# Kernel optimization log

Measured on AMD Instinct MI355X. Metric: run time of the kernel, lower is better.

## Reference

```python
import jax, jax.numpy as jnp
import numpy as np

B, M, D, H = 2, 2048, 1024, 16
DH = D // H            # 64 head dim
FF = 2624              # GeGLU intermediate size
EPS = 1e-5
ROPE_BASE = 10000.0


def _layernorm(x, g, b):
    mu = jnp.mean(x, axis=-1, keepdims=True)
    var = jnp.mean(jnp.square(x - mu), axis=-1, keepdims=True)
    return (x - mu) * jax.lax.rsqrt(var + EPS) * g + b


def _rope_cos_sin(m, dh):
    # HF-style: inv_freq over even dims; only first dh/2 entries are used by apply_rope
    inv_freq = 1.0 / (ROPE_BASE ** (jnp.arange(0, dh, 2, dtype=jnp.float32) / dh))  # [dh/2]
    ang = jnp.arange(m, dtype=jnp.float32)[:, None] * inv_freq[None, :]             # [M, dh/2]
    return jnp.cos(ang), jnp.sin(ang)


def _apply_rope(x, c, s):
    # x: [B,H,M,dh]; c,s: [M,dh/2] broadcast over B,H. Half-split (non-interleaved) rotation.
    x1, x2 = jnp.split(x, 2, axis=-1)
    return jnp.concatenate([x1 * c - x2 * s, x1 * s + x2 * c], axis=-1)


def setup_inputs() -> dict:
    key = jax.random.key(0)
    ks = jax.random.split(key, 6)
    w = lambda k, shape: (jax.random.normal(k, shape, jnp.float32) * 0.02)
    return {
        "hidden_states": jax.random.normal(ks[0], (B, M, D), jnp.float32),
        "attention_mask": jnp.ones((B, M), jnp.int32),
        "ln1_g": jnp.ones((D,), jnp.float32),
        "ln1_b": jnp.zeros((D,), jnp.float32),
        "Wqkv_w": w(ks[1], (3 * D, D)),
        "Wqkv_b": jnp.zeros((3 * D,), jnp.float32),
        "Wo_w": w(ks[2], (D, D)),
        "ln2_g": jnp.ones((D,), jnp.float32),
        "ln2_b": jnp.zeros((D,), jnp.float32),
        "Wi_w": w(ks[3], (2 * FF, D)),
        "Wmlp_o_w": w(ks[4], (D, FF)),
    }


def reference(hidden_states, attention_mask, ln1_g, ln1_b, Wqkv_w, Wqkv_b, Wo_w,
              ln2_g, ln2_b, Wi_w, Wmlp_o_w):
    x = hidden_states                                    # [B,M,D]
    xn = _layernorm(x, ln1_g, ln1_b)
    qkv = xn @ Wqkv_w.T + Wqkv_b                         # [B,M,3D]
    qkv = qkv.reshape(B, M, 3, H, DH).transpose(0, 3, 1, 2, 4)  # [B,H,M,3,dh]
    q, k, v = qkv[..., 0, :], qkv[..., 1, :], qkv[..., 2, :]    # each [B,H,M,dh]

    c, s = _rope_cos_sin(M, DH)                          # [M, dh/2]
    q = _apply_rope(q, c, s)
    k = _apply_rope(k, c, s)

    scale = 1.0 / np.sqrt(DH)
    scores = jnp.einsum("bhmd,bhnd->bhmn", q, k) * scale  # [B,H,M,M]
    keep = (attention_mask > 0)[:, None, None, :]         # [B,1,1,M] padding mask on keys
    scores = jnp.where(keep, scores, -jnp.inf)
    p = jax.nn.softmax(scores, axis=-1)
    o = jnp.einsum("bhmn,bhnd->bhmd", p, v)               # [B,H,M,dh]

    attn_out = o.transpose(0, 2, 1, 3).reshape(B, M, D)
    x = x + attn_out @ Wo_w.T

    # ModernBERT GeGLU MLP: input, gate = Wi(x).chunk(2); Wo(gelu(input) * gate)
    xn2 = _layernorm(x, ln2_g, ln2_b)
    hg = xn2 @ Wi_w.T                                     # [B,M,2*FF]
    h_in, h_gate = jnp.split(hg, 2, axis=-1)
    x = x + (jax.nn.gelu(h_in) * h_gate) @ Wmlp_o_w.T
    return x
```

## Files before the change

kernel.cpp:

```cpp
#include <hip/hip_runtime.h>
#include <cstdint>
#include <cstddef>

using u16 = unsigned short;
using u32 = uint32_t;

typedef __attribute__((ext_vector_type(8))) short short8;
typedef __attribute__((ext_vector_type(4))) float floatx4;

#define DEVFN static __device__ __forceinline__

#define QSCALE 0.18033688011112042f

DEVFN u16 f2bf(float f) {
  u32 u = __float_as_uint(f);
  return (u16)((u + 0x7fffu + ((u >> 16) & 1u)) >> 16);
}

DEVFN float b2f(u16 u) { return __uint_as_float(((u32)u) << 16); }

DEVFN void async_load16(const void* g, const void* lds) {
  __builtin_amdgcn_global_load_lds(
      (const __attribute__((address_space(1))) u32*)(uintptr_t)g,
      (__attribute__((address_space(3))) u32*)(u32)(uintptr_t)lds,
      16, 0, 0);
}

DEVFN void cvt4(const float* __restrict__ src, u16* __restrict__ dst, int i) {
  const float4 v = ((const float4*)src)[i];
  ushort4 o;
  o.x = f2bf(v.x); o.y = f2bf(v.y); o.z = f2bf(v.z); o.w = f2bf(v.w);
  ((ushort4*)dst)[i] = o;
}

__global__ __launch_bounds__(256)
void prep_k(const float* __restrict__ Wqkv, const float* __restrict__ Wo,
            const float* __restrict__ Wi, const float* __restrict__ Wmlp,
            const float* __restrict__ hidden, const float* __restrict__ ln1g,
            const float* __restrict__ ln1b,
            u16* __restrict__ wqkv_bf, u16* __restrict__ wo_bf,
            u16* __restrict__ wi_bf, u16* __restrict__ wmlp_bf,
            float* __restrict__ ct, float* __restrict__ st, u16* __restrict__ xn) {
  const int bid = blockIdx.x;
  const int tid = threadIdx.x;
  __shared__ float red[8];
  if (bid < 256) {
    const int i = bid * 256 + tid;
    const int m = i >> 5, f = i & 31;
    const float inv = exp2f((float)f * -0.41524101186092025f);
    const float ang = (float)m * inv;
    ct[i] = cosf(ang);
    st[i] = sinf(ang);
  } else if (bid < 3328) {
    cvt4(Wqkv, wqkv_bf, (bid - 256) * 256 + tid);
  } else if (bid < 4352) {
    cvt4(Wo, wo_bf, (bid - 3328) * 256 + tid);
  } else if (bid < 9600) {
    const int i = (bid - 4352) * 256 + tid;
    const int i4 = i * 4;
    const int p = i4 >> 10, kc = i4 & 1023;
    const int g = p >> 5, c = p & 31;
    const int srow = (c < 16) ? (g * 16 + c) : (2624 + g * 16 + (c - 16));
    const float4 v = *(const float4*)(Wi + (size_t)srow * 1024 + kc);
    ushort4 o;
    o.x = f2bf(v.x); o.y = f2bf(v.y); o.z = f2bf(v.z); o.w = f2bf(v.w);
    ((ushort4*)wi_bf)[i] = o;
  } else if (bid < 12224) {
    cvt4(Wmlp, wmlp_bf, (bid - 9600) * 256 + tid);
  } else {
    const int row = bid - 12224;
    const float4 v = ((const float4*)(hidden + (size_t)row * 1024))[tid];
    float s = v.x + v.y + v.z + v.w;
    float ss = v.x * v.x + v.y * v.y + v.z * v.z + v.w * v.w;
#pragma unroll
    for (int d = 32; d > 0; d >>= 1) {
      s += __shfl_xor(s, d);
      ss += __shfl_xor(ss, d);
    }
    const int wave = tid >> 6;
    if ((tid & 63) == 0) { red[wave] = s; red[4 + wave] = ss; }
    __syncthreads();
    s = red[0] + red[1] + red[2] + red[3];
    ss = red[4] + red[5] + red[6] + red[7];
    const float mu = s * (1.f / 1024.f);
    const float var = ss * (1.f / 1024.f) - mu * mu;
    const float rr = rsqrtf(var + 1e-5f);
    const float4 gv = ((const float4*)ln1g)[tid];
    const float4 bv = ((const float4*)ln1b)[tid];
    u16* orow = xn + (size_t)row * 1024 + tid * 4;
    orow[0] = f2bf((v.x - mu) * rr * gv.x + bv.x);
    orow[1] = f2bf((v.y - mu) * rr * gv.y + bv.y);
    orow[2] = f2bf((v.z - mu) * rr * gv.z + bv.z);
    orow[3] = f2bf((v.w - mu) * rr * gv.w + bv.w);
  }
}

__global__ __launch_bounds__(256)
void red_ln_k(const float* __restrict__ resid, const u16* __restrict__ p0,
              const u16* __restrict__ p1, const u16* __restrict__ p2,
              const float* __restrict__ g, const float* __restrict__ bb,
              float* __restrict__ outx, u16* __restrict__ outn) {
  const int row = blockIdx.x;
  const int tid = threadIdx.x;
  const size_t base = (size_t)row * 1024;
  const float4 h = ((const float4*)(resid + base))[tid];
  const ushort4 a = ((const ushort4*)(p0 + base))[tid];
  const ushort4 c = ((const ushort4*)(p1 + base))[tid];
  const ushort4 d = ((const ushort4*)(p2 + base))[tid];
  float4 v;
  v.x = h.x + b2f(a.x) + b2f(c.x) + b2f(d.x);
  v.y = h.y + b2f(a.y) + b2f(c.y) + b2f(d.y);
  v.z = h.z + b2f(a.z) + b2f(c.z) + b2f(d.z);
  v.w = h.w + b2f(a.w) + b2f(c.w) + b2f(d.w);
  float s = v.x + v.y + v.z + v.w;
  float ss = v.x * v.x + v.y * v.y + v.z * v.z + v.w * v.w;
#pragma unroll
  for (int dd = 32; dd > 0; dd >>= 1) {
    s += __shfl_xor(s, dd);
    ss += __shfl_xor(ss, dd);
  }
  __shared__ float red[8];
  const int wave = tid >> 6;
  if ((tid & 63) == 0) { red[wave] = s; red[4 + wave] = ss; }
  __syncthreads();
  s = red[0] + red[1] + red[2] + red[3];
  ss = red[4] + red[5] + red[6] + red[7];
  const float mu = s * (1.f / 1024.f);
  const float var = ss * (1.f / 1024.f) - mu * mu;
  const float rr = rsqrtf(var + 1e-5f);
  ((float4*)(outx + base))[tid] = v;
  const float4 gv = ((const float4*)g)[tid];
  const float4 bv = ((const float4*)bb)[tid];
  u16* orow = outn + base + tid * 4;
  orow[0] = f2bf((v.x - mu) * rr * gv.x + bv.x);
  orow[1] = f2bf((v.y - mu) * rr * gv.y + bv.y);
  orow[2] = f2bf((v.z - mu) * rr * gv.z + bv.z);
  orow[3] = f2bf((v.w - mu) * rr * gv.w + bv.w);
}

__global__ void red_add_k(float* __restrict__ out, const u16* __restrict__ p0,
                          const u16* __restrict__ p1, const u16* __restrict__ p2,
                          const u16* __restrict__ p3) {
  const int i = blockIdx.x * 256 + threadIdx.x;
  float4 v = ((const float4*)out)[i];
  const ushort4 a = ((const ushort4*)p0)[i];
  const ushort4 c = ((const ushort4*)p1)[i];
  const ushort4 d = ((const ushort4*)p2)[i];
  const ushort4 e = ((const ushort4*)p3)[i];
  v.x += b2f(a.x) + b2f(c.x) + b2f(d.x) + b2f(e.x);
  v.y += b2f(a.y) + b2f(c.y) + b2f(d.y) + b2f(e.y);
  v.z += b2f(a.z) + b2f(c.z) + b2f(d.z) + b2f(e.z);
  v.w += b2f(a.w) + b2f(c.w) + b2f(d.w) + b2f(e.w);
  ((float4*)out)[i] = v;
}

DEVFN void swizzle_tile(int NT, int& tn, int& tm) {
  const int tpx = gridDim.x >> 3;
  const int p = blockIdx.x;
  const int lid = (p & 7) * tpx + (p >> 3);
  const int band = lid / (8 * NT);
  const int rem = lid - band * 8 * NT;
  tn = (rem >> 3) * 128;
  tm = (band * 8 + (rem & 7)) * 128;
}

struct EpiArgs {
  const float* bias;
  u16* q; u16* kk; u16* vt;
  u16* outbf;
  const float* ct; const float* st;
};

template <int EPI>
__global__ __launch_bounds__(256, 3)
void gemm_k(const u16* __restrict__ A, const u16* __restrict__ B, int K, int NT,
            EpiArgs ea) {
  __shared__ __align__(16) u16 sA[128 * 32];
  __shared__ __align__(16) u16 sB[128 * 32];
  int tn, tm;
  swizzle_tile(NT, tn, tm);
  const int tid = threadIdx.x;
  const int wave = tid >> 6, lane = tid & 63;
  const int quad = lane >> 4, l15 = lane & 15;
  const int wm = (wave >> 1) * 64, wn = (wave & 1) * 64;

  floatx4 acc[4][4];
#pragma unroll
  for (int i = 0; i < 4; ++i)
#pragma unroll
    for (int j = 0; j < 4; ++j) acc[i][j] = (floatx4){0.f, 0.f, 0.f, 0.f};

  const int srow = lane >> 2;
  const int skc = (lane & 3) * 8;
  const u16* sAr = sA + (wm + l15) * 32 + quad * 8;
  const u16* sBr = sB + (wn + l15) * 32 + quad * 8;

  for (int k0 = 0; k0 < K; k0 += 32) {
#pragma unroll
    for (int j = 0; j < 2; ++j) {
      const int q = wave * 2 + j;
      const int row = q * 16 + srow;
      async_load16(A + (size_t)(tm + row) * K + (k0 + skc), (const char*)sA + q * 1024);
      async_load16(B + (size_t)(tn + row) * K + (k0 + skc), (const char*)sB + q * 1024);
    }
    __syncthreads();
    short8 af[4], bfr[4];
#pragma unroll
    for (int t = 0; t < 4; ++t) af[t] = *(const short8*)(sAr + t * 512);
#pragma unroll
    for (int t = 0; t < 4; ++t) bfr[t] = *(const short8*)(sBr + t * 512);
#pragma unroll
    for (int ti = 0; ti < 4; ++ti)
#pragma unroll
      for (int tj = 0; tj < 4; ++tj)
        acc[ti][tj] = __builtin_amdgcn_mfma_f32_16x16x32_bf16(af[ti], bfr[tj], acc[ti][tj], 0, 0, 0);
    __syncthreads();
  }

  if constexpr (EPI == 0) {
    const int col0 = tn + wn;
    const int t = col0 >> 10;
    const int h = (col0 & 1023) >> 6;
    if (t == 2) {
#pragma unroll
      for (int ti = 0; ti < 4; ++ti)
#pragma unroll
        for (int r = 0; r < 4; ++r) {
          const int row = tm + wm + ti * 16 + quad * 4 + r;
          const int b = row >> 11, m = row & 2047;
          const int mp = (m & ~31) | ((m & 15) << 1) | ((m >> 4) & 1);
#pragma unroll
          for (int tj = 0; tj < 4; ++tj) {
            const int dh = tj * 16 + l15;
            const float v = acc[ti][tj][r] + ea.bias[col0 + dh];
            ea.vt[((size_t)((b * 16 + h) * 64 + dh)) * 2048 + mp] = f2bf(v);
          }
        }
    } else {
      u16* dst = (t == 0) ? ea.q : ea.kk;
      const float qs = (t == 0) ? QSCALE : 1.f;
#pragma unroll
      for (int ti = 0; ti < 4; ++ti)
#pragma unroll
        for (int r = 0; r < 4; ++r) {
          const int row = tm + wm + ti * 16 + quad * 4 + r;
          const int b = row >> 11, m = row & 2047;
          u16* drow = dst + ((size_t)(b * 16 + h) * 2048 + m) * 64;
#pragma unroll
          for (int tj = 0; tj < 2; ++tj) {
            const int i = tj * 16 + l15;
            const float x1 = acc[ti][tj][r] + ea.bias[col0 + i];
            const float x2 = acc[ti][tj + 2][r] + ea.bias[col0 + 32 + i];
            const float cs = ea.ct[m * 32 + i];
            const float sn = ea.st[m * 32 + i];
            drow[i] = f2bf((x1 * cs - x2 * sn) * qs);
            drow[32 + i] = f2bf((x1 * sn + x2 * cs) * qs);
          }
        }
    }
  } else {
#pragma unroll
    for (int ti = 0; ti < 4; ++ti)
#pragma unroll
      for (int r = 0; r < 4; ++r) {
        const int row = tm + wm + ti * 16 + quad * 4 + r;
#pragma unroll
        for (int u = 0; u < 2; ++u) {
          const float hin = acc[ti][2 * u][r];
          const float hg = acc[ti][2 * u + 1][r];
          const int a = (((tn + wn) >> 5) + u) * 16 + l15;
          const float t2 = hin + 0.044715f * hin * hin * hin;
          const float e = __builtin_amdgcn_exp2f(t2 * -2.302114768f);
          const float gl = hin * __builtin_amdgcn_rcpf(1.f + e);
          ea.outbf[(size_t)row * 2624 + a] = f2bf(gl * hg);
        }
      }
  }
}

__global__ __launch_bounds__(256, 3)
void gemm_sk4(const u16* __restrict__ A, const u16* __restrict__ B, int K, int NT,
              int kps1, int zsw, int kps2,
              u16* __restrict__ p0, u16* __restrict__ p1,
              u16* __restrict__ p2, u16* __restrict__ p3) {
  __shared__ __align__(16) u16 sA[128 * 32];
  __shared__ __align__(16) u16 sB[128 * 32];
  int tn, tm;
  swizzle_tile(NT, tn, tm);
  const int z = blockIdx.y;
  int kofs, kps;
  if (z < zsw) { kofs = z * kps1; kps = kps1; }
  else { kofs = zsw * kps1 + (z - zsw) * kps2; kps = kps2; }
  const int tid = threadIdx.x;
  const int wave = tid >> 6, lane = tid & 63;
  const int quad = lane >> 4, l15 = lane & 15;
  const int wm = (wave >> 1) * 64, wn = (wave & 1) * 64;

  floatx4 acc[4][4];
#pragma unroll
  for (int i = 0; i < 4; ++i)
#pragma unroll
    for (int j = 0; j < 4; ++j) acc[i][j] = (floatx4){0.f, 0.f, 0.f, 0.f};

  const int srow = lane >> 2;
  const int skc = (lane & 3) * 8;
  const u16* sAr = sA + (wm + l15) * 32 + quad * 8;
  const u16* sBr = sB + (wn + l15) * 32 + quad * 8;

  for (int k0 = 0; k0 < kps; k0 += 32) {
    const int kk = kofs + k0;
#pragma unroll
    for (int j = 0; j < 2; ++j) {
      const int q = wave * 2 + j;
      const int row = q * 16 + srow;
      async_load16(A + (size_t)(tm + row) * K + (kk + skc), (const char*)sA + q * 1024);
      async_load16(B + (size_t)(tn + row) * K + (kk + skc), (const char*)sB + q * 1024);
    }
    __syncthreads();
    short8 af[4], bfr[4];
#pragma unroll
    for (int t = 0; t < 4; ++t) af[t] = *(const short8*)(sAr + t * 512);
#pragma unroll
    for (int t = 0; t < 4; ++t) bfr[t] = *(const short8*)(sBr + t * 512);
#pragma unroll
    for (int ti = 0; ti < 4; ++ti)
#pragma unroll
      for (int tj = 0; tj < 4; ++tj)
        acc[ti][tj] = __builtin_amdgcn_mfma_f32_16x16x32_bf16(af[ti], bfr[tj], acc[ti][tj], 0, 0, 0);
    __syncthreads();
  }

  u16* part = (z == 0) ? p0 : (z == 1) ? p1 : (z == 2) ? p2 : p3;
#pragma unroll
  for (int ti = 0; ti < 4; ++ti)
#pragma unroll
    for (int r = 0; r < 4; ++r) {
      const int row = tm + wm + ti * 16 + quad * 4 + r;
#pragma unroll
      for (int tj = 0; tj < 4; ++tj)
        part[(size_t)row * 1024 + tn + wn + tj * 16 + l15] = f2bf(acc[ti][tj][r]);
    }
}

DEVFN void attn_stage(const u16* __restrict__ kg, const u16* __restrict__ vtg,
                      size_t bhbase_k, size_t bhbase_v, int key0, int wave,
                      int lane, const u16* sK, const u16* sV) {
#pragma unroll
  for (int j = 0; j < 8; ++j) {
    const int qi = wave * 8 + j;
    if (qi < 16) {
      const int chunk = qi >> 1, half = qi & 1;
      const int row = half * 64 + lane;
      async_load16(kg + bhbase_k + (size_t)(key0 + row) * 64 + chunk * 8,
                   (const char*)sK + qi * 1024);
    } else {
      const int vi = qi - 16;
      const int c = vi >> 2, kc = vi & 3;
      async_load16(vtg + bhbase_v + (size_t)lane * 2048 + key0 + c * 32 + kc * 8,
                   (const char*)sV + vi * 1024);
    }
  }
}

__global__ __launch_bounds__(256, 2)
void attn_k(const u16* __restrict__ qg, const u16* __restrict__ kg,
            const u16* __restrict__ vtg, const int* __restrict__ mask,
            u16* __restrict__ outg) {
  __shared__ __align__(16) u16 sKV[2][16384];
  __shared__ __align__(16) u16 sP[8 * 16 * 40];
  const int bh = blockIdx.y;
  const int b = bh >> 4, h = bh & 15;
  const int q0 = blockIdx.x * 128;
  const int tid = threadIdx.x;
  const int wave = tid >> 6, lane = tid & 63;
  const int quad = lane >> 4, l15 = lane & 15;
  const size_t bhk = (size_t)bh * 2048 * 64;
  const size_t bhv = (size_t)bh * 64 * 2048;

  short8 aq[2][2];
#pragma unroll
  for (int g = 0; g < 2; ++g) {
    const u16* qptr = qg + ((size_t)bh * 2048 + q0 + wave * 32 + g * 16 + l15) * 64 + quad * 8;
    aq[g][0] = *(const short8*)qptr;
    aq[g][1] = *(const short8*)(qptr + 32);
  }

  floatx4 o[2][4];
#pragma unroll
  for (int g = 0; g < 2; ++g)
#pragma unroll
    for (int t = 0; t < 4; ++t) o[g][t] = (floatx4){0.f, 0.f, 0.f, 0.f};
  float li[2][4] = {{0.f, 0.f, 0.f, 0.f}, {0.f, 0.f, 0.f, 0.f}};
  const floatx4 z4 = {0.f, 0.f, 0.f, 0.f};

  float mbc[8];
#pragma unroll
  for (int tj = 0; tj < 8; ++tj)
    mbc[tj] = (mask[b * 2048 + tj * 16 + l15] > 0) ? 0.f : -1e30f;

  attn_stage(kg, vtg, bhk, bhv, 0, wave, lane, sKV[0], sKV[0] + 8192);
  __syncthreads();

  int buf = 0;
  for (int kt = 0; kt < 16; ++kt) {
    const u16* sK = sKV[buf];
    const u16* sV = sKV[buf] + 8192;
    float mbn[8];
    if (kt < 15) {
      attn_stage(kg, vtg, bhk, bhv, (kt + 1) * 128, wave, lane,
                 sKV[buf ^ 1], sKV[buf ^ 1] + 8192);
#pragma unroll
      for (int tj = 0; tj < 8; ++tj)
        mbn[tj] = (mask[b * 2048 + (kt + 1) * 128 + tj * 16 + l15] > 0) ? 0.f : -1e30f;
    }

    floatx4 sacc[2][8];
#pragma unroll
    for (int tj = 0; tj < 8; ++tj) {
      const short8 b0 = *(const short8*)(sK + quad * 1024 + (tj * 16 + l15) * 8);
      const short8 b1 = *(const short8*)(sK + (4 + quad) * 1024 + (tj * 16 + l15) * 8);
      sacc[0][tj] = __builtin_amdgcn_mfma_f32_16x16x32_bf16(aq[0][0], b0, z4, 0, 0, 0);
      sacc[0][tj] = __builtin_amdgcn_mfma_f32_16x16x32_bf16(aq[0][1], b1, sacc[0][tj], 0, 0, 0);
      sacc[1][tj] = __builtin_amdgcn_mfma_f32_16x16x32_bf16(aq[1][0], b0, z4, 0, 0, 0);
      sacc[1][tj] = __builtin_amdgcn_mfma_f32_16x16x32_bf16(aq[1][1], b1, sacc[1][tj], 0, 0, 0);
    }

#pragma unroll
    for (int g = 0; g < 2; ++g)
#pragma unroll
      for (int r = 0; r < 4; ++r) {
        float sum = li[g][r];
#pragma unroll
        for (int tj = 0; tj < 8; ++tj) {
          const float p = __builtin_amdgcn_exp2f(sacc[g][tj][r] + mbc[tj]);
          sacc[g][tj][r] = p;
          sum += p;
        }
        li[g][r] = sum;
      }

#pragma unroll
    for (int c = 0; c < 4; ++c) {
#pragma unroll
      for (int g = 0; g < 2; ++g) {
        u32* pw32 = (u32*)sP + (wave * 2 + g) * 320;
#pragma unroll
        for (int r = 0; r < 4; ++r) {
          const u32 lo = __float_as_uint(sacc[g][c * 2][r]) + 0x8000u;
          const u32 hi = __float_as_uint(sacc[g][c * 2 + 1][r]) + 0x8000u;
          pw32[(quad * 4 + r) * 20 + l15] = __builtin_amdgcn_perm(hi, lo, 0x07060302);
        }
      }
      asm volatile("s_waitcnt lgkmcnt(0)" ::: "memory");
      short8 ap[2];
#pragma unroll
      for (int g = 0; g < 2; ++g)
        ap[g] = *(const short8*)(sP + (wave * 2 + g) * 640 + l15 * 40 + quad * 8);
#pragma unroll
      for (int tj2 = 0; tj2 < 4; ++tj2) {
        const short8 bv = *(const short8*)(sV + (c * 4 + quad) * 512 + (tj2 * 16 + l15) * 8);
        o[0][tj2] = __builtin_amdgcn_mfma_f32_16x16x32_bf16(ap[0], bv, o[0][tj2], 0, 0, 0);
        o[1][tj2] = __builtin_amdgcn_mfma_f32_16x16x32_bf16(ap[1], bv, o[1][tj2], 0, 0, 0);
      }
    }
    __syncthreads();
#pragma unroll
    for (int tj = 0; tj < 8; ++tj) mbc[tj] = mbn[tj];
    buf ^= 1;
  }

#pragma unroll
  for (int g = 0; g < 2; ++g)
#pragma unroll
    for (int r = 0; r < 4; ++r) {
      float s = li[g][r];
      s += __shfl_xor(s, 1);
      s += __shfl_xor(s, 2);
      s += __shfl_xor(s, 4);
      s += __shfl_xor(s, 8);
      li[g][r] = 1.f / s;
    }

#pragma unroll
  for (int g = 0; g < 2; ++g)
#pragma unroll
    for (int tj = 0; tj < 4; ++tj)
#pragma unroll
      for (int r = 0; r < 4; ++r) {
        const int m = q0 + wave * 32 + g * 16 + quad * 4 + r;
        outg[((size_t)b * 2048 + m) * 1024 + h * 64 + tj * 16 + l15] =
            f2bf(o[g][tj][r] * li[g][r]);
      }
}

static const size_t OFF_WQKV = 0;
static const size_t OFF_WO   = 6291456;
static const size_t OFF_WI   = 8388608;
static const size_t OFF_WMLP = 19136512;
static const size_t OFF_XN   = 24510464;
static const size_t OFF_Q    = 32899072;
static const size_t OFF_K    = 41287680;
static const size_t OFF_VT   = 49676288;
static const size_t OFF_ATT  = 58064896;
static const size_t OFF_ROPE = OFF_ATT;
static const size_t WS_NEED  = 66453504;

extern "C" void kernel_launch(void* const* d_in, const int* in_sizes, int n_in,
                              void* d_out, int out_size, void* d_ws, size_t ws_size,
                              hipStream_t stream) {
  (void)in_sizes; (void)n_in; (void)out_size;
  if (ws_size < WS_NEED) return;

  const float* hidden = (const float*)d_in[0];
  const int*   mask   = (const int*)d_in[1];
  const float* ln1g   = (const float*)d_in[2];
  const float* ln1b   = (const float*)d_in[3];
  const float* Wqkv   = (const float*)d_in[4];
  const float* Wqkvb  = (const float*)d_in[5];
  const float* Wo     = (const float*)d_in[6];
  const float* ln2g   = (const float*)d_in[7];
  const float* ln2b   = (const float*)d_in[8];
  const float* Wi     = (const float*)d_in[9];
  const float* Wmlp   = (const float*)d_in[10];
  float* out = (float*)d_out;
  char* ws = (char*)d_ws;

  u16* wqkv_bf = (u16*)(ws + OFF_WQKV);
  u16* wo_bf   = (u16*)(ws + OFF_WO);
  u16* wi_bf   = (u16*)(ws + OFF_WI);
  u16* wmlp_bf = (u16*)(ws + OFF_WMLP);
  u16* xn      = (u16*)(ws + OFF_XN);
  u16* qb      = (u16*)(ws + OFF_Q);
  u16* kb      = (u16*)(ws + OFF_K);
  u16* vtb     = (u16*)(ws + OFF_VT);
  u16* att     = (u16*)(ws + OFF_ATT);
  u16* act     = (u16*)(ws + OFF_Q);
  float* ct    = (float*)(ws + OFF_ROPE);
  float* st    = (float*)(ws + OFF_ROPE + 262144);
  u16* wp0     = (u16*)(ws + OFF_Q);
  u16* wp1     = (u16*)(ws + OFF_K);
  u16* wp2     = (u16*)(ws + OFF_VT);
  u16* mp0     = (u16*)(ws + OFF_XN);
  u16* mp1     = (u16*)(ws + OFF_ATT);
  u16* mp2     = (u16*)(ws + OFF_WI);
  u16* mp3     = (u16*)(ws + OFF_WQKV);

  prep_k<<<16320, 256, 0, stream>>>(Wqkv, Wo, Wi, Wmlp, hidden, ln1g, ln1b,
                                    wqkv_bf, wo_bf, wi_bf, wmlp_bf, ct, st, xn);

  EpiArgs e1 = {Wqkvb, qb, kb, vtb, nullptr, ct, st};
  gemm_k<0><<<768, 256, 0, stream>>>(xn, wqkv_bf, 1024, 24, e1);

  attn_k<<<dim3(16, 32), 256, 0, stream>>>(qb, kb, vtb, mask, att);

  gemm_sk4<<<dim3(256, 3), 256, 0, stream>>>(att, wo_bf, 1024, 8, 352, 2, 320,
                                             wp0, wp1, wp2, wp2);
  red_ln_k<<<4096, 256, 0, stream>>>(hidden, wp0, wp1, wp2, ln2g, ln2b, out, xn);

  EpiArgs e3 = {nullptr, nullptr, nullptr, nullptr, act, nullptr, nullptr};
  gemm_k<2><<<1312, 256, 0, stream>>>(xn, wi_bf, 1024, 41, e3);

  gemm_sk4<<<dim3(256, 4), 256, 0, stream>>>(act, wmlp_bf, 2624, 8, 672, 2, 640,
                                             mp0, mp1, mp2, mp3);
  red_add_k<<<4096, 256, 0, stream>>>(out, mp0, mp1, mp2, mp3);
}
```

Baseline: 354.5 us.

## Load V directly from global into registers, add mask fast path and setprio

```diff
diff --git a/kernel.cpp b/kernel.cpp
--- a/kernel.cpp
+++ b/kernel.cpp
@@ -342,23 +342,15 @@
     }
 }
 
-DEVFN void attn_stage(const u16* __restrict__ kg, const u16* __restrict__ vtg,
-                      size_t bhbase_k, size_t bhbase_v, int key0, int wave,
-                      int lane, const u16* sK, const u16* sV) {
-#pragma unroll
-  for (int j = 0; j < 8; ++j) {
-    const int qi = wave * 8 + j;
-    if (qi < 16) {
-      const int chunk = qi >> 1, half = qi & 1;
-      const int row = half * 64 + lane;
-      async_load16(kg + bhbase_k + (size_t)(key0 + row) * 64 + chunk * 8,
-                   (const char*)sK + qi * 1024);
-    } else {
-      const int vi = qi - 16;
-      const int c = vi >> 2, kc = vi & 3;
-      async_load16(vtg + bhbase_v + (size_t)lane * 2048 + key0 + c * 32 + kc * 8,
-                   (const char*)sV + vi * 1024);
-    }
+DEVFN void attn_stage(const u16* __restrict__ kg, size_t bhbase_k, int key0,
+                      int wave, int lane, const u16* sK) {
+#pragma unroll
+  for (int j = 0; j < 4; ++j) {
+    const int qi = wave * 4 + j;
+    const int chunk = qi >> 1, half = qi & 1;
+    const int row = half * 64 + lane;
+    async_load16(kg + bhbase_k + (size_t)(key0 + row) * 64 + chunk * 8,
+                 (const char*)sK + qi * 1024);
   }
 }
 
@@ -366,7 +358,7 @@
 void attn_k(const u16* __restrict__ qg, const u16* __restrict__ kg,
             const u16* __restrict__ vtg, const int* __restrict__ mask,
             u16* __restrict__ outg) {
-  __shared__ __align__(16) u16 sKV[2][16384];
+  __shared__ __align__(16) u16 sK2[2][8192];
   __shared__ __align__(16) u16 sP[8 * 16 * 40];
   const int bh = blockIdx.y;
   const int b = bh >> 4, h = bh & 15;
@@ -393,28 +385,30 @@
   float li[2][4] = {{0.f, 0.f, 0.f, 0.f}, {0.f, 0.f, 0.f, 0.f}};
   const floatx4 z4 = {0.f, 0.f, 0.f, 0.f};
 
+  const u16* vbase = vtg + bhv + (size_t)l15 * 2048 + quad * 8;
+
   float mbc[8];
 #pragma unroll
   for (int tj = 0; tj < 8; ++tj)
     mbc[tj] = (mask[b * 2048 + tj * 16 + l15] > 0) ? 0.f : -1e30f;
 
-  attn_stage(kg, vtg, bhk, bhv, 0, wave, lane, sKV[0], sKV[0] + 8192);
+  attn_stage(kg, bhk, 0, wave, lane, sK2[0]);
   __syncthreads();
 
   int buf = 0;
   for (int kt = 0; kt < 16; ++kt) {
-    const u16* sK = sKV[buf];
-    const u16* sV = sKV[buf] + 8192;
+    const u16* sK = sK2[buf];
+    const int key0 = kt * 128;
     float mbn[8];
     if (kt < 15) {
-      attn_stage(kg, vtg, bhk, bhv, (kt + 1) * 128, wave, lane,
-                 sKV[buf ^ 1], sKV[buf ^ 1] + 8192);
+      attn_stage(kg, bhk, key0 + 128, wave, lane, sK2[buf ^ 1]);
 #pragma unroll
       for (int tj = 0; tj < 8; ++tj)
-        mbn[tj] = (mask[b * 2048 + (kt + 1) * 128 + tj * 16 + l15] > 0) ? 0.f : -1e30f;
+        mbn[tj] = (mask[b * 2048 + key0 + 128 + tj * 16 + l15] > 0) ? 0.f : -1e30f;
     }
 
     floatx4 sacc[2][8];
+    __builtin_amdgcn_s_setprio(1);
 #pragma unroll
     for (int tj = 0; tj < 8; ++tj) {
       const short8 b0 = *(const short8*)(sK + quad * 1024 + (tj * 16 + l15) * 8);
@@ -424,20 +418,45 @@
       sacc[1][tj] = __builtin_amdgcn_mfma_f32_16x16x32_bf16(aq[1][0], b0, z4, 0, 0, 0);
       sacc[1][tj] = __builtin_amdgcn_mfma_f32_16x16x32_bf16(aq[1][1], b1, sacc[1][tj], 0, 0, 0);
     }
-
-#pragma unroll
-    for (int g = 0; g < 2; ++g)
-#pragma unroll
-      for (int r = 0; r < 4; ++r) {
-        float sum = li[g][r];
-#pragma unroll
-        for (int tj = 0; tj < 8; ++tj) {
-          const float p = __builtin_amdgcn_exp2f(sacc[g][tj][r] + mbc[tj]);
-          sacc[g][tj][r] = p;
-          sum += p;
+    __builtin_amdgcn_s_setprio(0);
+
+    short8 bv[4][4];
+    const u16* vb = vbase + key0;
+#pragma unroll
+    for (int t = 0; t < 4; ++t) bv[0][t] = *(const short8*)(vb + (size_t)t * 32768);
+#pragma unroll
+    for (int t = 0; t < 4; ++t) bv[1][t] = *(const short8*)(vb + (size_t)t * 32768 + 32);
+
+    const float msum = mbc[0] + mbc[1] + mbc[2] + mbc[3] + mbc[4] + mbc[5] + mbc[6] + mbc[7];
+    if (__all(msum == 0.f)) {
+#pragma unroll
+      for (int g = 0; g < 2; ++g)
+#pragma unroll
+        for (int r = 0; r < 4; ++r) {
+          float sum = li[g][r];
+#pragma unroll
+          for (int tj = 0; tj < 8; ++tj) {
+            const float p = __builtin_amdgcn_exp2f(sacc[g][tj][r]);
+            sacc[g][tj][r] = p;
+            sum += p;
+          }
+          li[g][r] = sum;
         }
-        li[g][r] = sum;
-      }
+    } else {
+#pragma unroll
+      for (int g = 0; g < 2; ++g)
+#pragma unroll
+        for (int r = 0; r < 4; ++r) {
+          float sum = li[g][r];
+#pragma unroll
+          for (int tj = 0; tj < 8; ++tj) {
+            const float p = __builtin_amdgcn_exp2f(sacc[g][tj][r] + mbc[tj]);
+            sacc[g][tj][r] = p;
+            sum += p;
+          }
+          li[g][r] = sum;
+        }
+    }
 
 #pragma unroll
     for (int c = 0; c < 4; ++c) {
@@ -456,12 +475,21 @@
 #pragma unroll
       for (int g = 0; g < 2; ++g)
         ap[g] = *(const short8*)(sP + (wave * 2 + g) * 640 + l15 * 40 + quad * 8);
+      if (c == 0) {
+#pragma unroll
+        for (int t = 0; t < 4; ++t) bv[2][t] = *(const short8*)(vb + (size_t)t * 32768 + 64);
+      }
+      if (c == 1) {
+#pragma unroll
+        for (int t = 0; t < 4; ++t) bv[3][t] = *(const short8*)(vb + (size_t)t * 32768 + 96);
+      }
+      __builtin_amdgcn_s_setprio(1);
 #pragma unroll
       for (int tj2 = 0; tj2 < 4; ++tj2) {
-        const short8 bv = *(const short8*)(sV + (c * 4 + quad) * 512 + (tj2 * 16 + l15) * 8);
-        o[0][tj2] = __builtin_amdgcn_mfma_f32_16x16x32_bf16(ap[0], bv, o[0][tj2], 0, 0, 0);
-        o[1][tj2] = __builtin_amdgcn_mfma_f32_16x16x32_bf16(ap[1], bv, o[1][tj2], 0, 0, 0);
+        o[0][tj2] = __builtin_amdgcn_mfma_f32_16x16x32_bf16(ap[0], bv[c][tj2], o[0][tj2], 0, 0, 0);
+        o[1][tj2] = __builtin_amdgcn_mfma_f32_16x16x32_bf16(ap[1], bv[c][tj2], o[1][tj2], 0, 0, 0);
       }
+      __builtin_amdgcn_s_setprio(0);
     }
     __syncthreads();
 #pragma unroll
```

Result: slower. 366.6 us (+3.4%).

## Shrink attention tiles to 64 queries/keys, remap blocks per XCD, add mask fast path

Applied to the files above, without the earlier changes.

```diff
diff --git a/kernel.cpp b/kernel.cpp
--- a/kernel.cpp
+++ b/kernel.cpp
@@ -342,155 +342,157 @@
     }
 }
 
-DEVFN void attn_stage(const u16* __restrict__ kg, const u16* __restrict__ vtg,
-                      size_t bhbase_k, size_t bhbase_v, int key0, int wave,
-                      int lane, const u16* sK, const u16* sV) {
-#pragma unroll
-  for (int j = 0; j < 8; ++j) {
-    const int qi = wave * 8 + j;
-    if (qi < 16) {
-      const int chunk = qi >> 1, half = qi & 1;
-      const int row = half * 64 + lane;
-      async_load16(kg + bhbase_k + (size_t)(key0 + row) * 64 + chunk * 8,
+DEVFN void attn_stage64(const u16* __restrict__ kg, const u16* __restrict__ vtg,
+                        size_t bhk, size_t bhv, int key0, int wave, int lane,
+                        const u16* sK, const u16* sV) {
+#pragma unroll
+  for (int j = 0; j < 4; ++j) {
+    const int qi = wave * 4 + j;
+    if (qi < 8) {
+      async_load16(kg + bhk + (size_t)(key0 + lane) * 64 + qi * 8,
                    (const char*)sK + qi * 1024);
     } else {
-      const int vi = qi - 16;
+      const int vi = qi - 8;
       const int c = vi >> 2, kc = vi & 3;
-      async_load16(vtg + bhbase_v + (size_t)lane * 2048 + key0 + c * 32 + kc * 8,
+      async_load16(vtg + bhv + (size_t)lane * 2048 + key0 + c * 32 + kc * 8,
                    (const char*)sV + vi * 1024);
     }
   }
 }
 
-__global__ __launch_bounds__(256, 2)
+__global__ __launch_bounds__(256, 4)
 void attn_k(const u16* __restrict__ qg, const u16* __restrict__ kg,
             const u16* __restrict__ vtg, const int* __restrict__ mask,
             u16* __restrict__ outg) {
-  __shared__ __align__(16) u16 sKV[2][16384];
-  __shared__ __align__(16) u16 sP[8 * 16 * 40];
-  const int bh = blockIdx.y;
+  __shared__ __align__(16) u16 sKV[2][8192];
+  __shared__ __align__(16) u16 sP[4 * 16 * 40];
+  const int L = blockIdx.x;
+  const int xcd = L & 7, idx = L >> 3;
+  const int bh = (xcd << 2) | (idx >> 5);
+  const int q0 = (idx & 31) * 64;
   const int b = bh >> 4, h = bh & 15;
-  const int q0 = blockIdx.x * 128;
   const int tid = threadIdx.x;
   const int wave = tid >> 6, lane = tid & 63;
   const int quad = lane >> 4, l15 = lane & 15;
   const size_t bhk = (size_t)bh * 2048 * 64;
   const size_t bhv = (size_t)bh * 64 * 2048;
 
-  short8 aq[2][2];
-#pragma unroll
-  for (int g = 0; g < 2; ++g) {
-    const u16* qptr = qg + ((size_t)bh * 2048 + q0 + wave * 32 + g * 16 + l15) * 64 + quad * 8;
-    aq[g][0] = *(const short8*)qptr;
-    aq[g][1] = *(const short8*)(qptr + 32);
-  }
-
-  floatx4 o[2][4];
-#pragma unroll
-  for (int g = 0; g < 2; ++g)
-#pragma unroll
-    for (int t = 0; t < 4; ++t) o[g][t] = (floatx4){0.f, 0.f, 0.f, 0.f};
-  float li[2][4] = {{0.f, 0.f, 0.f, 0.f}, {0.f, 0.f, 0.f, 0.f}};
+  short8 aq[2];
+  {
+    const u16* qptr = qg + ((size_t)bh * 2048 + q0 + wave * 16 + l15) * 64 + quad * 8;
+    aq[0] = *(const short8*)qptr;
+    aq[1] = *(const short8*)(qptr + 32);
+  }
+
+  floatx4 o[4];
+#pragma unroll
+  for (int t = 0; t < 4; ++t) o[t] = (floatx4){0.f, 0.f, 0.f, 0.f};
+  float li[4] = {0.f, 0.f, 0.f, 0.f};
   const floatx4 z4 = {0.f, 0.f, 0.f, 0.f};
 
-  float mbc[8];
-#pragma unroll
-  for (int tj = 0; tj < 8; ++tj)
+  float mbc[4];
+#pragma unroll
+  for (int tj = 0; tj < 4; ++tj)
     mbc[tj] = (mask[b * 2048 + tj * 16 + l15] > 0) ? 0.f : -1e30f;
 
-  attn_stage(kg, vtg, bhk, bhv, 0, wave, lane, sKV[0], sKV[0] + 8192);
+  attn_stage64(kg, vtg, bhk, bhv, 0, wave, lane, sKV[0], sKV[0] + 4096);
   __syncthreads();
 
   int buf = 0;
-  for (int kt = 0; kt < 16; ++kt) {
+  for (int kt = 0; kt < 32; ++kt) {
     const u16* sK = sKV[buf];
-    const u16* sV = sKV[buf] + 8192;
-    float mbn[8];
-    if (kt < 15) {
-      attn_stage(kg, vtg, bhk, bhv, (kt + 1) * 128, wave, lane,
-                 sKV[buf ^ 1], sKV[buf ^ 1] + 8192);
-#pragma unroll
-      for (int tj = 0; tj < 8; ++tj)
-        mbn[tj] = (mask[b * 2048 + (kt + 1) * 128 + tj * 16 + l15] > 0) ? 0.f : -1e30f;
-    }
-
-    floatx4 sacc[2][8];
-#pragma unroll
-    for (int tj = 0; tj < 8; ++tj) {
-      const short8 b0 = *(const short8*)(sK + quad * 1024 + (tj * 16 + l15) * 8);
-      const short8 b1 = *(const short8*)(sK + (4 + quad) * 1024 + (tj * 16 + l15) * 8);
-      sacc[0][tj] = __builtin_amdgcn_mfma_f32_16x16x32_bf16(aq[0][0], b0, z4, 0, 0, 0);
-      sacc[0][tj] = __builtin_amdgcn_mfma_f32_16x16x32_bf16(aq[0][1], b1, sacc[0][tj], 0, 0, 0);
-      sacc[1][tj] = __builtin_amdgcn_mfma_f32_16x16x32_bf16(aq[1][0], b0, z4, 0, 0, 0);
-      sacc[1][tj] = __builtin_amdgcn_mfma_f32_16x16x32_bf16(aq[1][1], b1, sacc[1][tj], 0, 0, 0);
-    }
-
-#pragma unroll
-    for (int g = 0; g < 2; ++g)
+    const u16* sV = sKV[buf] + 4096;
+    const int key0 = kt * 64;
+    float mbn[4];
+    if (kt < 31) {
+      attn_stage64(kg, vtg, bhk, bhv, key0 + 64, wave, lane,
+                   sKV[buf ^ 1], sKV[buf ^ 1] + 4096);
+#pragma unroll
+      for (int tj = 0; tj < 4; ++tj)
+        mbn[tj] = (mask[b * 2048 + key0 + 64 + tj * 16 + l15] > 0) ? 0.f : -1e30f;
+    }
+
+    floatx4 sacc[4];
+    __builtin_amdgcn_s_setprio(1);
+#pragma unroll
+    for (int tj = 0; tj < 4; ++tj) {
+      const short8 b0 = *(const short8*)(sK + quad * 512 + (tj * 16 + l15) * 8);
+      const short8 b1 = *(const short8*)(sK + (4 + quad) * 512 + (tj * 16 + l15) * 8);
+      sacc[tj] = __builtin_amdgcn_mfma_f32_16x16x32_bf16(aq[0], b0, z4, 0, 0, 0);
+      sacc[tj] = __builtin_amdgcn_mfma_f32_16x16x32_bf16(aq[1], b1, sacc[tj], 0, 0, 0);
+    }
+    __builtin_amdgcn_s_setprio(0);
+
+    const float msum = mbc[0] + mbc[1] + mbc[2] + mbc[3];
+    if (__all(msum == 0.f)) {
 #pragma unroll
       for (int r = 0; r < 4; ++r) {
-        float sum = li[g][r];
-#pragma unroll
-        for (int tj = 0; tj < 8; ++tj) {
-          const float p = __builtin_amdgcn_exp2f(sacc[g][tj][r] + mbc[tj]);
-          sacc[g][tj][r] = p;
+        float sum = li[r];
+#pragma unroll
+        for (int tj = 0; tj < 4; ++tj) {
+          const float p = __builtin_amdgcn_exp2f(sacc[tj][r]);
+          sacc[tj][r] = p;
           sum += p;
         }
-        li[g][r] = sum;
+        li[r] = sum;
       }
-
-#pragma unroll
-    for (int c = 0; c < 4; ++c) {
-#pragma unroll
-      for (int g = 0; g < 2; ++g) {
-        u32* pw32 = (u32*)sP + (wave * 2 + g) * 320;
-#pragma unroll
-        for (int r = 0; r < 4; ++r) {
-          const u32 lo = __float_as_uint(sacc[g][c * 2][r]) + 0x8000u;
-          const u32 hi = __float_as_uint(sacc[g][c * 2 + 1][r]) + 0x8000u;
-          pw32[(quad * 4 + r) * 20 + l15] = __builtin_amdgcn_perm(hi, lo, 0x07060302);
+    } else {
+#pragma unroll
+      for (int r = 0; r < 4; ++r) {
+        float sum = li[r];
+#pragma unroll
+        for (int tj = 0; tj < 4; ++tj) {
+          const float p = __builtin_amdgcn_exp2f(sacc[tj][r] + mbc[tj]);
+          sacc[tj][r] = p;
+          sum += p;
         }
+        li[r] = sum;
+      }
+    }
+
+#pragma unroll
+    for (int c = 0; c < 2; ++c) {
+      u32* pw32 = (u32*)sP + wave * 320;
+#pragma unroll
+      for (int r = 0; r < 4; ++r) {
+        const u32 lo = __float_as_uint(sacc[c * 2][r]) + 0x8000u;
+        const u32 hi = __float_as_uint(sacc[c * 2 + 1][r]) + 0x8000u;
+        pw32[(quad * 4 + r) * 20 + l15] = __builtin_amdgcn_perm(hi, lo, 0x07060302);
       }
       asm volatile("s_waitcnt lgkmcnt(0)" ::: "memory");
-      short8 ap[2];
-#pragma unroll
-      for (int g = 0; g < 2; ++g)
-        ap[g] = *(const short8*)(sP + (wave * 2 + g) * 640 + l15 * 40 + quad * 8);
+      const short8 ap = *(const short8*)(sP + wave * 640 + l15 * 40 + quad * 8);
+      __builtin_amdgcn_s_setprio(1);
 #pragma unroll
       for (int tj2 = 0; tj2 < 4; ++tj2) {
         const short8 bv = *(const short8*)(sV + (c * 4 + quad) * 512 + (tj2 * 16 + l15) * 8);
-        o[0][tj2] = __builtin_amdgcn_mfma_f32_16x16x32_bf16(ap[0], bv, o[0][tj2], 0, 0, 0);
-        o[1][tj2] = __builtin_amdgcn_mfma_f32_16x16x32_bf16(ap[1], bv, o[1][tj2], 0, 0, 0);
+        o[tj2] = __builtin_amdgcn_mfma_f32_16x16x32_bf16(ap, bv, o[tj2], 0, 0, 0);
       }
+      __builtin_amdgcn_s_setprio(0);
     }
     __syncthreads();
 #pragma unroll
-    for (int tj = 0; tj < 8; ++tj) mbc[tj] = mbn[tj];
+    for (int tj = 0; tj < 4; ++tj) mbc[tj] = mbn[tj];
     buf ^= 1;
   }
 
 #pragma unroll
-  for (int g = 0; g < 2; ++g)
+  for (int r = 0; r < 4; ++r) {
+    float s = li[r];
+    s += __shfl_xor(s, 1);
+    s += __shfl_xor(s, 2);
+    s += __shfl_xor(s, 4);
+    s += __shfl_xor(s, 8);
+    li[r] = 1.f / s;
+  }
+
+#pragma unroll
+  for (int tj = 0; tj < 4; ++tj)
 #pragma unroll
     for (int r = 0; r < 4; ++r) {
-      float s = li[g][r];
-      s += __shfl_xor(s, 1);
-      s += __shfl_xor(s, 2);
-      s += __shfl_xor(s, 4);
-      s += __shfl_xor(s, 8);
-      li[g][r] = 1.f / s;
-    }
-
-#pragma unroll
-  for (int g = 0; g < 2; ++g)
-#pragma unroll
-    for (int tj = 0; tj < 4; ++tj)
-#pragma unroll
-      for (int r = 0; r < 4; ++r) {
-        const int m = q0 + wave * 32 + g * 16 + quad * 4 + r;
-        outg[((size_t)b * 2048 + m) * 1024 + h * 64 + tj * 16 + l15] =
-            f2bf(o[g][tj][r] * li[g][r]);
-      }
+      const int m = q0 + wave * 16 + quad * 4 + r;
+      outg[((size_t)b * 2048 + m) * 1024 + h * 64 + tj * 16 + l15] =
+          f2bf(o[tj][r] * li[r]);
+    }
 }
 
 static const size_t OFF_WQKV = 0;
@@ -551,7 +553,7 @@
   EpiArgs e1 = {Wqkvb, qb, kb, vtb, nullptr, ct, st};
   gemm_k<0><<<768, 256, 0, stream>>>(xn, wqkv_bf, 1024, 24, e1);
 
-  attn_k<<<dim3(16, 32), 256, 0, stream>>>(qb, kb, vtb, mask, att);
+  attn_k<<<dim3(1024), 256, 0, stream>>>(qb, kb, vtb, mask, att);
 
   gemm_sk4<<<dim3(256, 3), 256, 0, stream>>>(att, wo_bf, 1024, 8, 352, 2, 320,
                                              wp0, wp1, wp2, wp2);
```

Measured after the change: 358.1 us. Within noise of the previous version (+1.0%).
